# Performance work log

Measured on AMD Instinct MI355X. Metric: run time of the kernel, lower is better.

## Reference

```python
import jax, jax.numpy as jnp
import numpy as np

B, S, E, R = 64, 2048, 256, 50


def setup_inputs() -> dict:
    key = jax.random.key(0)
    ks = jax.random.split(key, 22)
    n = lambda k, shp, s=0.05: (jax.random.normal(k, shp, jnp.float32) * s)
    d = {
        "encoder_o": jax.random.normal(ks[0], (B, S, E), jnp.float32),
        "h0": jax.random.normal(ks[1], (1, B, E), jnp.float32),
        "c0": jax.random.normal(ks[2], (1, B, E), jnp.float32),
        "r_in": jax.random.randint(ks[3], (B,), 0, R),
        "k1": jax.random.randint(ks[4], (B, 1), 0, S),
        "k2": jax.random.randint(ks[5], (B, 1), 0, S),
        "W_ih": n(ks[6], (4 * E, E)),
        "W_hh": n(ks[7], (4 * E, E)),
        "b_ih": n(ks[8], (4 * E,)),
        "b_hh": n(ks[9], (4 * E,)),
        "W_attn": n(ks[10], (E, 2 * E)),
        "b_attn": n(ks[11], (E,)),
        "W_conv": n(ks[12], (E, 2 * E, 3)),
        "b_conv": n(ks[13], (E,)),
        "sos_emb": n(ks[14], (1, E)),
        "rel_emb": n(ks[15], (R, E)),
        "W_rel": n(ks[16], (R, E)),
        "b_rel": n(ks[17], (R,)),
        "W_ent1": n(ks[18], (1, E)),
        "b_ent1": n(ks[19], (1,)),
        "W_ent2": n(ks[20], (1, E)),
        "b_ent2": n(ks[21], (1,)),
    }
    return d


def reference(encoder_o, h0, c0, r_in, k1, k2, W_ih, W_hh, b_ih, b_hh,
              W_attn, b_attn, W_conv, b_conv, sos_emb, rel_emb,
              W_rel, b_rel, W_ent1, b_ent1, W_ent2, b_ent2):
    Bx, Sx, Ex = encoder_o.shape

    def lstm_step(x, h, c):  # single decode step, x/h/c: [B,E]
        gates = x @ W_ih.T + h @ W_hh.T + (b_ih + b_hh)  # [B,4E]
        i, f, g, o = jnp.split(gates, 4, axis=-1)        # PyTorch gate order i,f,g,o
        c2 = jax.nn.sigmoid(f) * c + jax.nn.sigmoid(i) * jnp.tanh(g)
        h2 = jax.nn.sigmoid(o) * jnp.tanh(c2)
        return h2, c2

    def attend(q):  # Luong dot attention + tanh(linear(cat(mix,q))); q: [B,E]
        scores = jnp.einsum('be,bse->bs', q, encoder_o)
        attn = jax.nn.softmax(scores, axis=-1)
        mix = jnp.einsum('bs,bse->be', attn, encoder_o)
        comb = jnp.concatenate([mix, q], axis=-1)        # [B,2E]
        return jnp.tanh(comb @ W_attn.T + b_attn)

    def step(x, h, c):
        h2, c2 = lstm_step(x, h, c)
        return attend(h2), h2, c2

    kern = jnp.transpose(W_conv, (2, 1, 0))  # [3, 2E, E] for NWC/WIO

    def ent_heads(o):  # o: [B,E]
        vec = jnp.broadcast_to(o[:, None, :], (Bx, Sx, Ex))  # seq_and_vec
        feat = jnp.concatenate([encoder_o, vec], axis=-1)    # [B,S,2E]
        conv = jax.lax.conv_general_dilated(
            feat, kern, (1,), 'SAME',
            dimension_numbers=('NWC', 'WIO', 'NWC')) + b_conv
        conv = jax.nn.relu(conv)                             # [B,S,E]
        e1 = conv @ W_ent1.T + b_ent1                        # [B,S,1]
        e2 = conv @ W_ent2.T + b_ent2
        return e1, e2

    h, c = h0[0], c0[0]
    # t1: <sos> -> relation logits
    x = jnp.broadcast_to(sos_emb[0], (Bx, Ex))
    out1, h, c = step(x, h, c)
    t1_out = out1 @ W_rel.T + b_rel                          # [B,R]
    # t2: relation embedding -> entity-1 span heads
    out2, h, c = step(rel_emb[r_in], h, c)
    e1a, e2a = ent_heads(out2)
    # t3: gathered k1+k2 encoder vectors -> entity-2 span heads
    idx = jnp.arange(Bx)
    kk = encoder_o[idx, k1[:, 0]] + encoder_o[idx, k2[:, 0]]  # vectorized seq_gather
    out3, h, c = step(kk, h, c)
    e1b, e2b = ent_heads(out3)
    # pack outputs: [B, R + 4*S]
    return jnp.concatenate(
        [t1_out, e1a[..., 0], e2a[..., 0], e1b[..., 0], e2b[..., 0]], axis=1)
```

## Files before the change

### kernel.cpp

```cpp
#include <hip/hip_runtime.h>
#include <hip/hip_bf16.h>

#define EE 256
#define SS 2048
#define BB 64
#define RN 50
#define OSTR 8242
#define NCH 16

typedef __attribute__((ext_vector_type(4))) float vf4;
typedef __attribute__((ext_vector_type(8))) short s8v;
typedef __attribute__((ext_vector_type(4))) short s4v;
typedef __attribute__((ext_vector_type(4))) unsigned short u16x4;
typedef __attribute__((ext_vector_type(2))) unsigned int u32x2;
typedef __attribute__((ext_vector_type(4))) unsigned int u32x4;

__device__ __forceinline__ unsigned short f2bf(float f){
  __hip_bfloat16 h = __float2bfloat16(f);
  return *reinterpret_cast<unsigned short*>(&h);
}
__device__ __forceinline__ unsigned int f2bf2(float a, float b){
  __hip_bfloat162 h = __float22bfloat162_rn(make_float2(a, b));
  return *reinterpret_cast<unsigned int*>(&h);
}
__device__ __forceinline__ float sigm(float x){ return 1.0f/(1.0f + __expf(-x)); }
__device__ __forceinline__ float dot4(vf4 a, vf4 b){ return a.x*b.x + a.y*b.y + a.z*b.z + a.w*b.w; }

__device__ __forceinline__ vf4 mfma16(s4v a, s4v b, vf4 c){
#if __has_builtin(__builtin_amdgcn_mfma_f32_16x16x16bf16_1k)
  return __builtin_amdgcn_mfma_f32_16x16x16bf16_1k(a, b, c, 0, 0, 0);
#else
  vf4 d;
  asm volatile("v_mfma_f32_16x16x16_bf16 %0, %1, %2, %3\n\ts_nop 7\n\ts_nop 7"
               : "=v"(d) : "v"(a), "v"(b), "v"(c));
  return d;
#endif
}

__device__ __forceinline__ void gload_lds16(const void* g, void* l){
  __builtin_amdgcn_global_load_lds(
      (const __attribute__((address_space(1))) unsigned int*)g,
      (__attribute__((address_space(3))) unsigned int*)l, 16, 0, 0);
}

__global__ __launch_bounds__(256) void k_prep(
  const float* __restrict__ enc, const float* __restrict__ h0, const float* __restrict__ c0,
  const int* __restrict__ r_in, const int* __restrict__ k1, const int* __restrict__ k2,
  const float* __restrict__ sos, const float* __restrict__ rel,
  const float* __restrict__ W_conv,
  float* __restrict__ xT, float* __restrict__ hT0, float* __restrict__ cT,
  unsigned short* __restrict__ WT, unsigned short* __restrict__ Bp)
{
  int bid = blockIdx.x, t = threadIdx.x;
  if (bid < 256){
    int part = bid >> 6, b = bid & 63;
    if (part == 0){
      xT[(size_t)0*EE*BB + t*BB + b] = sos[t];
    } else if (part == 1){
      xT[(size_t)1*EE*BB + t*BB + b] = rel[r_in[b]*EE + t];
    } else if (part == 2){
      int i1 = k1[b], i2 = k2[b];
      xT[(size_t)2*EE*BB + t*BB + b] =
        enc[((size_t)b*SS + i1)*EE + t] + enc[((size_t)b*SS + i2)*EE + t];
    } else {
      hT0[t*BB + b] = h0[b*EE + t];
      cT [t*BB + b] = c0[b*EE + t];
    }
  } else if (bid < 512){
    int o = bid - 256;
    for (int r = t; r < 768; r += 256)
      WT[(size_t)r*EE + o] = f2bf(W_conv[(size_t)o*1536 + 768 + r]);
  } else {
    int gid = (bid - 512)*256 + t;
    int kc  = gid >> 10;
    int rem = gid & 1023;
    int ni  = rem >> 6;
    int l   = rem & 63;
    int o   = ni*16 + (l & 15);
    int kbase = kc*32 + ((l >> 4) << 3);
    u16x4 lo4, hi4;
    #pragma unroll
    for (int j=0;j<8;++j){
      int k = kbase + j; int ktap = k >> 8; int i = k & 255;
      unsigned short v = f2bf(W_conv[((size_t)o*512 + i)*3 + ktap]);
      if (j<4){ if(j==0)lo4.x=v; else if(j==1)lo4.y=v; else if(j==2)lo4.z=v; else lo4.w=v; }
      else    { if(j==4)hi4.x=v; else if(j==5)hi4.y=v; else if(j==6)hi4.z=v; else hi4.w=v; }
    }
    u16x4* dst = (u16x4*)(Bp + (size_t)gid*8);
    dst[0] = lo4; dst[1] = hi4;
  }
}

__global__ __launch_bounds__(1024) void k_step(
  const float* __restrict__ hT_cur, const float* __restrict__ xT_st,
  const float* __restrict__ W_ih, const float* __restrict__ W_hh,
  const float* __restrict__ b_ih, const float* __restrict__ b_hh,
  float* __restrict__ cT, float* __restrict__ hT_next, float* __restrict__ hs_st)
{
  int e = blockIdx.x, tid = threadIdx.x;
  int w = tid >> 6, b = tid & 63;
  int g = w & 3, kq = w >> 2;
  int grow = g*EE + e;
  const float* wh = W_hh + (size_t)grow*EE + kq*64;
  const float* wi = W_ih + (size_t)grow*EE + kq*64;
  const float* hT = hT_cur + kq*64*BB;
  const float* xv = xT_st + kq*64*BB;
  float acc = (kq == 0) ? (b_ih[grow] + b_hh[grow]) : 0.0f;
  #pragma unroll 4
  for (int k4 = 0; k4 < 16; ++k4){
    vf4 wh4 = *(const vf4*)(wh + k4*4);
    vf4 wi4 = *(const vf4*)(wi + k4*4);
    int k = k4*4;
    acc += hT[(k+0)*BB+b]*wh4.x + hT[(k+1)*BB+b]*wh4.y
         + hT[(k+2)*BB+b]*wh4.z + hT[(k+3)*BB+b]*wh4.w;
    acc += xv[(k+0)*BB+b]*wi4.x + xv[(k+1)*BB+b]*wi4.y
         + xv[(k+2)*BB+b]*wi4.z + xv[(k+3)*BB+b]*wi4.w;
  }
  __shared__ float sm[16][BB];
  sm[w][b] = acc;
  __syncthreads();
  if (tid < BB){
    float iv = sm[0][tid]+sm[4][tid]+sm[8][tid] +sm[12][tid];
    float fv = sm[1][tid]+sm[5][tid]+sm[9][tid] +sm[13][tid];
    float gv = sm[2][tid]+sm[6][tid]+sm[10][tid]+sm[14][tid];
    float ov = sm[3][tid]+sm[7][tid]+sm[11][tid]+sm[15][tid];
    float cprev = cT[e*BB + tid];
    float cn = sigm(fv)*cprev + sigm(iv)*tanhf(gv);
    float hn = sigm(ov)*tanhf(cn);
    cT[e*BB + tid] = cn;
    hT_next[e*BB + tid] = hn;
    hs_st[(size_t)tid*EE + e] = hn;
  }
}

__global__ __launch_bounds__(256) void k_attend(
  const float* __restrict__ enc, const float* __restrict__ hs,
  float* __restrict__ mixc, float* __restrict__ stats,
  unsigned short* __restrict__ encb)
{
  int bid = blockIdx.x; int b = bid >> 4, ch = bid & 15;
  int tid = threadIdx.x, lane = tid & 63, wv = tid >> 6;
  __shared__ float sc[3][128];
  __shared__ vf4 mpart[4][3][64];

  const float* chunk = enc + ((size_t)b*SS + ch*128)*EE;

  {
    int rs = lane >> 4, cg = lane & 15;
    vf4 q0[4], q1[4], q2[4];
    #pragma unroll
    for (int v=0; v<4; ++v){
      q0[v] = *(const vf4*)(hs + ((size_t)0*BB + b)*EE + cg*16 + v*4);
      q1[v] = *(const vf4*)(hs + ((size_t)1*BB + b)*EE + cg*16 + v*4);
      q2[v] = *(const vf4*)(hs + ((size_t)2*BB + b)*EE + cg*16 + v*4);
    }
    #pragma unroll
    for (int i=0; i<8; ++i){
      int r = wv*32 + i*4 + rs;
      const vf4* rp = (const vf4*)(chunk + (size_t)r*EE + cg*16);
      vf4 e0v = rp[0], e1v = rp[1], e2v = rp[2], e3v = rp[3];
      float a0 = dot4(e0v,q0[0]) + dot4(e1v,q0[1]) + dot4(e2v,q0[2]) + dot4(e3v,q0[3]);
      float a1 = dot4(e0v,q1[0]) + dot4(e1v,q1[1]) + dot4(e2v,q1[2]) + dot4(e3v,q1[3]);
      float a2 = dot4(e0v,q2[0]) + dot4(e1v,q2[1]) + dot4(e2v,q2[2]) + dot4(e3v,q2[3]);
      if (encb){
        int gs = ch*128 + r;
        int key = ((gs + 1) & 7) << 4;
        char* base = (char*)encb + ((size_t)b*SS + gs)*512;
        u32x4 p1; p1.x = f2bf2(e0v.x,e0v.y); p1.y = f2bf2(e0v.z,e0v.w);
                  p1.z = f2bf2(e1v.x,e1v.y); p1.w = f2bf2(e1v.z,e1v.w);
        u32x4 p2; p2.x = f2bf2(e2v.x,e2v.y); p2.y = f2bf2(e2v.z,e2v.w);
                  p2.z = f2bf2(e3v.x,e3v.y); p2.w = f2bf2(e3v.z,e3v.w);
        *(u32x4*)(base + ((cg*32     ) ^ key)) = p1;
        *(u32x4*)(base + ((cg*32 + 16) ^ key)) = p2;
      }
      #pragma unroll
      for (int d=1; d<16; d<<=1){
        a0 += __shfl_xor(a0,d); a1 += __shfl_xor(a1,d); a2 += __shfl_xor(a2,d);
      }
      if (cg == 0){ sc[0][r]=a0; sc[1][r]=a1; sc[2][r]=a2; }
    }
  }
  __syncthreads();

  if (tid < 64){
    float s0a = sc[0][tid], s0b = sc[0][64+tid];
    float s1a = sc[1][tid], s1b = sc[1][64+tid];
    float s2a = sc[2][tid], s2b = sc[2][64+tid];
    float m0 = fmaxf(s0a,s0b), m1 = fmaxf(s1a,s1b), m2 = fmaxf(s2a,s2b);
    #pragma unroll
    for (int d=1; d<64; d<<=1){
      m0 = fmaxf(m0, __shfl_xor(m0,d));
      m1 = fmaxf(m1, __shfl_xor(m1,d));
      m2 = fmaxf(m2, __shfl_xor(m2,d));
    }
    float e0a = __expf(s0a-m0), e0b = __expf(s0b-m0);
    float e1a = __expf(s1a-m1), e1b = __expf(s1b-m1);
    float e2a = __expf(s2a-m2), e2b = __expf(s2b-m2);
    sc[0][tid]=e0a; sc[0][64+tid]=e0b;
    sc[1][tid]=e1a; sc[1][64+tid]=e1b;
    sc[2][tid]=e2a; sc[2][64+tid]=e2b;
    float l0=e0a+e0b, l1=e1a+e1b, l2=e2a+e2b;
    #pragma unroll
    for (int d=1; d<64; d<<=1){
      l0 += __shfl_xor(l0,d); l1 += __shfl_xor(l1,d); l2 += __shfl_xor(l2,d);
    }
    if (tid == 0){
      int o0 = ((0*BB+b)*NCH + ch)*2; stats[o0]=m0; stats[o0+1]=l0;
      int o1 = ((1*BB+b)*NCH + ch)*2; stats[o1]=m1; stats[o1+1]=l1;
      int o2 = ((2*BB+b)*NCH + ch)*2; stats[o2]=m2; stats[o2+1]=l2;
    }
  }
  __syncthreads();

  {
    vf4 A0 = (vf4)0.0f, A1 = (vf4)0.0f, A2 = (vf4)0.0f;
    #pragma unroll 4
    for (int j=0;j<32;++j){
      int r = wv*32 + j;
      int gs = ch*128 + r;
      vf4 ev;
      if (encb){
        int key = ((gs + 1) & 7) << 4;
        u32x2 pk = *(const u32x2*)((const char*)encb + ((size_t)b*SS + gs)*512 + ((lane*8) ^ key));
        ev.x = __uint_as_float(pk.x << 16);
        ev.y = __uint_as_float(pk.x & 0xFFFF0000u);
        ev.z = __uint_as_float(pk.y << 16);
        ev.w = __uint_as_float(pk.y & 0xFFFF0000u);
      } else {
        ev = *(const vf4*)(chunk + (size_t)r*EE + lane*4);
      }
      float w0 = sc[0][r], w1 = sc[1][r], w2 = sc[2][r];
      A0 += ev*w0; A1 += ev*w1; A2 += ev*w2;
    }
    mpart[wv][0][lane]=A0; mpart[wv][1][lane]=A1; mpart[wv][2][lane]=A2;
  }
  __syncthreads();
  if (tid < 192){
    int q = tid >> 6, e4 = tid & 63;
    vf4 sum = mpart[0][q][e4] + mpart[1][q][e4] + mpart[2][q][e4] + mpart[3][q][e4];
    *(vf4*)(mixc + ((size_t)(q*BB+b)*NCH + ch)*EE + e4*4) = sum;
  }
}

__global__ __launch_bounds__(256) void k_post(
  const float* __restrict__ mixc, const float* __restrict__ hs,
  const float* __restrict__ stats,
  const float* __restrict__ W_attn, const float* __restrict__ b_attn,
  const float* __restrict__ W_rel, const float* __restrict__ b_rel,
  const unsigned short* __restrict__ WT, const float* __restrict__ b_conv,
  float* __restrict__ out, float* __restrict__ vv)
{
  int b = blockIdx.x, t = threadIdx.x;
  __shared__ float comb[3][2*EE];
  __shared__ float o1[EE], o2s[EE], o3s[EE];
  #pragma unroll
  for (int q=0;q<3;q++){
    float M = -1e30f;
    for (int c=0;c<NCH;c++) M = fmaxf(M, stats[((q*BB+b)*NCH + c)*2]);
    float L = 0.f, macc = 0.f;
    for (int c=0;c<NCH;c++){
      int o = ((q*BB+b)*NCH + c)*2;
      float e = __expf(stats[o]-M);
      L += stats[o+1]*e;
      macc += mixc[((size_t)(q*BB+b)*NCH + c)*EE + t] * e;
    }
    comb[q][t] = macc / L;
    comb[q][EE+t] = hs[((size_t)q*BB + b)*EE + t];
  }
  __syncthreads();
  float a0 = b_attn[t], a1 = a0, a2 = a0;
  const vf4* wr = (const vf4*)(W_attn + (size_t)t*2*EE);
  const vf4* c0v = (const vf4*)comb[0];
  const vf4* c1v = (const vf4*)comb[1];
  const vf4* c2v = (const vf4*)comb[2];
  #pragma unroll 4
  for (int k=0;k<2*EE/4;++k){
    vf4 w = wr[k];
    a0 += dot4(w, c0v[k]); a1 += dot4(w, c1v[k]); a2 += dot4(w, c2v[k]);
  }
  o1[t]=tanhf(a0); o2s[t]=tanhf(a1); o3s[t]=tanhf(a2);
  __syncthreads();
  if (t < RN){
    float acc = b_rel[t];
    const vf4* wrel = (const vf4*)(W_rel + (size_t)t*EE);
    const vf4* ov = (const vf4*)o1;
    for (int k=0;k<EE/4;++k) acc += dot4(wrel[k], ov[k]);
    out[(size_t)b*OSTR + t] = acc;
  }
  float va0=0,va1=0,va2=0, vb0=0,vb1=0,vb2=0;
  for (int i=0;i<EE;++i){
    float x2 = o2s[i], x3 = o3s[i];
    const unsigned short* wt = WT + (size_t)i*3*EE + t;
    float w0 = __uint_as_float(((unsigned int)wt[0]) << 16);
    float w1 = __uint_as_float(((unsigned int)wt[EE]) << 16);
    float w2 = __uint_as_float(((unsigned int)wt[2*EE]) << 16);
    va0 += x2*w0; va1 += x2*w1; va2 += x2*w2;
    vb0 += x3*w0; vb1 += x3*w1; vb2 += x3*w2;
  }
  float bc = b_conv[t];
  vv[((0*3+0)*BB + b)*EE + t] = va0+va1+va2+bc;
  vv[((0*3+1)*BB + b)*EE + t] = va1+va2+bc;
  vv[((0*3+2)*BB + b)*EE + t] = va0+va1+bc;
  vv[((1*3+0)*BB + b)*EE + t] = vb0+vb1+vb2+bc;
  vv[((1*3+1)*BB + b)*EE + t] = vb1+vb2+bc;
  vv[((1*3+2)*BB + b)*EE + t] = vb0+vb1+bc;
}

__global__ __launch_bounds__(256, 3) void k_conv(
  const float* __restrict__ enc, const unsigned short* __restrict__ encb,
  const unsigned short* __restrict__ Bp,
  const float* __restrict__ vv,
  const float* __restrict__ W_e1, const float* __restrict__ b_e1,
  const float* __restrict__ W_e2, const float* __restrict__ b_e2,
  float* __restrict__ out)
{
  int stile = blockIdx.x, b = blockIdx.y;
  int s0 = stile*64;
  int tid = threadIdx.x, lane = tid & 63, w = tid >> 6;
  int lo = lane & 15, hi = lane >> 4;
  __shared__ __align__(16) unsigned short Ab[66*256];
  __shared__ float part2[4][64][4];

  if (encb){
    const char* ebase = (const char*)encb + (size_t)b*SS*512;
    for (int base = 0; base < 66*32; base += 256){
      int idx = base + tid;
      if (idx < 66*32){
        int r = idx >> 5, c = idx & 31;
        int srow = s0 - 1 + r;
        srow = srow < 0 ? 0 : (srow > SS-1 ? SS-1 : srow);
        gload_lds16(ebase + (size_t)srow*512 + c*16, (char*)Ab + idx*16);
      }
    }
    __syncthreads();
    if (stile == 0 || stile == 31){
      if (stile == 0  && tid < 32) *(vf4*)((char*)Ab + tid*16) = (vf4)0.0f;
      if (stile == 31 && tid < 32) *(vf4*)((char*)Ab + 65*512 + tid*16) = (vf4)0.0f;
      __syncthreads();
    }
  } else {
    const float* eb = enc + (size_t)b*SS*EE;
    for (int idx = tid; idx < 66*64; idx += 256){
      int r = idx >> 6, c4 = idx & 63;
      int s = s0 - 1 + r;
      vf4 v = (vf4)0.0f;
      if (s >= 0 && s < SS) v = *(const vf4*)(eb + (size_t)s*EE + c4*4);
      u32x2 pk; pk.x = f2bf2(v.x, v.y); pk.y = f2bf2(v.z, v.w);
      int byte = (r*512 + c4*8) ^ ((r & 7) << 4);
      *(u32x2*)((char*)Ab + byte) = pk;
    }
    __syncthreads();
  }

  vf4 acc[4][4];
  #pragma unroll
  for (int oi=0;oi<4;++oi){
    #pragma unroll
    for (int si=0;si<4;++si) acc[oi][si] = (vf4)0.0f;
  }
  const s8v* Bp8 = (const s8v*)Bp;
  s8v bf[4], bfn[4];
  #pragma unroll
  for (int oi=0;oi<4;++oi) bf[oi] = Bp8[((0*16 + (w*4+oi)) << 6) + lane];

  for (int kc=0; kc<24; ++kc){
    int ktap = kc >> 3;
    int colb = ((kc & 7) << 6) + (hi << 4);
    s8v af[4];
    #pragma unroll
    for (int si=0;si<4;++si){
      int row = si*16 + lo + ktap;
      int byte = row*512 + (colb ^ ((row & 7) << 4));
      af[si] = *(const s8v*)((const char*)Ab + byte);
    }
    if (kc < 23){
      #pragma unroll
      for (int oi=0;oi<4;++oi) bfn[oi] = Bp8[(((kc+1)*16 + (w*4+oi)) << 6) + lane];
    }
    #pragma unroll
    for (int oi=0;oi<4;++oi){
      #pragma unroll
      for (int si=0;si<4;++si)
        acc[oi][si] = __builtin_amdgcn_mfma_f32_16x16x32_bf16(bf[oi], af[si], acc[oi][si], 0, 0, 0);
    }
    #pragma unroll
    for (int oi=0;oi<4;++oi) bf[oi] = bfn[oi];
  }

  bool firstTile = (s0 == 0), lastTile = (s0 + 64 == SS);
  vf4 vaI[4], vbI[4]; s4v aw[4];
  #pragma unroll
  for (int oi=0;oi<4;++oi){
    int o4 = w*64 + oi*16 + hi*4;
    vaI[oi] = *(const vf4*)(vv + ((0*3+0)*BB + b)*EE + o4);
    vbI[oi] = *(const vf4*)(vv + ((1*3+0)*BB + b)*EE + o4);
    vf4 w1 = *(const vf4*)(W_e1 + o4);
    vf4 w2 = *(const vf4*)(W_e2 + o4);
    float e0 = (lo==0) ? w1.x : ((lo==1) ? w2.x : 0.0f);
    float e1 = (lo==0) ? w1.y : ((lo==1) ? w2.y : 0.0f);
    float e2 = (lo==0) ? w1.z : ((lo==1) ? w2.z : 0.0f);
    float e3 = (lo==0) ? w1.w : ((lo==1) ? w2.w : 0.0f);
    u32x2 t; t.x = f2bf2(e0, e1); t.y = f2bf2(e2, e3);
    aw[oi] = __builtin_bit_cast(s4v, t);
  }
  #pragma unroll
  for (int si=0; si<4; ++si){
    vf4 Da = (vf4)0.0f, Db = (vf4)0.0f;
    #pragma unroll
    for (int oi=0; oi<4; ++oi){
      int o4 = w*64 + oi*16 + hi*4;
      vf4 c = acc[oi][si];
      vf4 va = vaI[oi], vb = vbI[oi];
      if (firstTile && si==0 && lo==0){
        va = *(const vf4*)(vv + ((0*3+1)*BB + b)*EE + o4);
        vb = *(const vf4*)(vv + ((1*3+1)*BB + b)*EE + o4);
      }
      if (lastTile && si==3 && lo==15){
        va = *(const vf4*)(vv + ((0*3+2)*BB + b)*EE + o4);
        vb = *(const vf4*)(vv + ((1*3+2)*BB + b)*EE + o4);
      }
      float a0 = fmaxf(c.x+va.x,0.f), a1 = fmaxf(c.y+va.y,0.f);
      float a2 = fmaxf(c.z+va.z,0.f), a3 = fmaxf(c.w+va.w,0.f);
      float b0 = fmaxf(c.x+vb.x,0.f), b1 = fmaxf(c.y+vb.y,0.f);
      float b2 = fmaxf(c.z+vb.z,0.f), b3 = fmaxf(c.w+vb.w,0.f);
      u32x2 ta; ta.x = f2bf2(a0,a1); ta.y = f2bf2(a2,a3);
      u32x2 tb; tb.x = f2bf2(b0,b1); tb.y = f2bf2(b2,b3);
      Da = mfma16(aw[oi], __builtin_bit_cast(s4v, ta), Da);
      Db = mfma16(aw[oi], __builtin_bit_cast(s4v, tb), Db);
    }
    if (hi == 0){
      vf4 pk; pk.x = Da.x; pk.y = Da.y; pk.z = Db.x; pk.w = Db.y;
      *(vf4*)&part2[w][si*16+lo][0] = pk;
    }
  }
  __syncthreads();
  {
    int s = tid >> 2, c = tid & 3;
    float r = part2[0][s][c] + part2[1][s][c] + part2[2][s][c] + part2[3][s][c];
    r += (c & 1) ? b_e2[0] : b_e1[0];
    out[(size_t)b*OSTR + RN + c*SS + (s0 + s)] = r;
  }
}

extern "C" void kernel_launch(void* const* d_in, const int* in_sizes, int n_in,
                              void* d_out, int out_size, void* d_ws, size_t ws_size,
                              hipStream_t stream)
{
  const float* enc   = (const float*)d_in[0];
  const float* h0    = (const float*)d_in[1];
  const float* c0    = (const float*)d_in[2];
  const int*   r_in  = (const int*)d_in[3];
  const int*   k1    = (const int*)d_in[4];
  const int*   k2    = (const int*)d_in[5];
  const float* W_ih  = (const float*)d_in[6];
  const float* W_hh  = (const float*)d_in[7];
  const float* b_ih  = (const float*)d_in[8];
  const float* b_hh  = (const float*)d_in[9];
  const float* W_attn= (const float*)d_in[10];
  const float* b_attn= (const float*)d_in[11];
  const float* W_conv= (const float*)d_in[12];
  const float* b_conv= (const float*)d_in[13];
  const float* sos   = (const float*)d_in[14];
  const float* rel   = (const float*)d_in[15];
  const float* W_rel = (const float*)d_in[16];
  const float* b_rel = (const float*)d_in[17];
  const float* W_e1  = (const float*)d_in[18];
  const float* b_e1  = (const float*)d_in[19];
  const float* W_e2  = (const float*)d_in[20];
  const float* b_e2  = (const float*)d_in[21];
  float* out = (float*)d_out;
  char* ws = (char*)d_ws;

  float* hs    = (float*)(ws);
  float* vv    = (float*)(ws + 196608);
  float* stats = (float*)(ws + 589824);
  float* mixc  = (float*)(ws + 638976);
  unsigned short* Bp = (unsigned short*)(ws + 6930432);
  float* xT    = (float*)(ws + 7323648);
  float* hTa   = (float*)(ws + 7520256);
  float* hTb   = (float*)(ws + 7585792);
  float* cT    = (float*)(ws + 7651328);
  unsigned short* WT = (unsigned short*)(ws + 7716864);
  size_t encb_off = 8110080;
  size_t need = encb_off + (size_t)BB*SS*EE*2;
  unsigned short* encb = (ws_size >= need) ? (unsigned short*)(ws + encb_off) : nullptr;

  hipLaunchKernelGGL(k_prep,  dim3(608), dim3(256), 0, stream,
                     enc,h0,c0,r_in,k1,k2,sos,rel,W_conv, xT,hTa,cT, WT,Bp);
  hipLaunchKernelGGL(k_step,  dim3(256), dim3(1024), 0, stream,
                     hTa, xT + 0*EE*BB, W_ih,W_hh,b_ih,b_hh, cT, hTb, hs + 0*BB*EE);
  hipLaunchKernelGGL(k_step,  dim3(256), dim3(1024), 0, stream,
                     hTb, xT + 1*EE*BB, W_ih,W_hh,b_ih,b_hh, cT, hTa, hs + 1*BB*EE);
  hipLaunchKernelGGL(k_step,  dim3(256), dim3(1024), 0, stream,
                     hTa, xT + 2*EE*BB, W_ih,W_hh,b_ih,b_hh, cT, hTb, hs + 2*BB*EE);
  hipLaunchKernelGGL(k_attend,dim3(1024), dim3(256), 0, stream, enc, hs, mixc, stats, encb);
  hipLaunchKernelGGL(k_post,  dim3(64),  dim3(256), 0, stream,
                     mixc, hs, stats, W_attn,b_attn, W_rel,b_rel, WT, b_conv, out, vv);
  hipLaunchKernelGGL(k_conv,  dim3(32,64), dim3(256), 0, stream,
                     enc, encb, Bp, vv, W_e1,b_e1, W_e2,b_e2, out);
}
```

Baseline: 183.9 us.

## Split attention kernel into separate score and mix kernels

Splits the fused attention kernel into two kernels. The first computes the three query scores per position and writes them, together with the bf16 swizzled encoder copy, to global memory. The second reads the scores back, does the chunk softmax, and accumulates the mix from the bf16 copy. This removes the in-block barrier between scoring and mixing, but adds a kernel launch, a global round trip for the scores, and a second pass over the encoder data, which may now miss in cache.

```diff
diff --git a/kernel.cpp b/kernel.cpp
--- a/kernel.cpp
+++ b/kernel.cpp
@@ -133,59 +133,73 @@
   }
 }
 
-__global__ __launch_bounds__(256) void k_attend(
+__global__ __launch_bounds__(256) void k_score(
   const float* __restrict__ enc, const float* __restrict__ hs,
+  float* __restrict__ scw, unsigned short* __restrict__ encb)
+{
+  int bid = blockIdx.x; int b = bid >> 4, wg = bid & 15;
+  int tid = threadIdx.x, lane = tid & 63, wv = tid >> 6;
+  int rs = lane >> 4, cg = lane & 15;
+  int s0 = (wg*4 + wv)*32;
+  const float* chunk = enc + ((size_t)b*SS + s0)*EE;
+
+  vf4 q0[4], q1[4], q2[4];
+  #pragma unroll
+  for (int v=0; v<4; ++v){
+    q0[v] = *(const vf4*)(hs + ((size_t)0*BB + b)*EE + cg*16 + v*4);
+    q1[v] = *(const vf4*)(hs + ((size_t)1*BB + b)*EE + cg*16 + v*4);
+    q2[v] = *(const vf4*)(hs + ((size_t)2*BB + b)*EE + cg*16 + v*4);
+  }
+  #pragma unroll
+  for (int i=0; i<8; ++i){
+    int r = i*4 + rs;
+    const vf4* rp = (const vf4*)(chunk + (size_t)r*EE + cg*16);
+    vf4 e0v = rp[0], e1v = rp[1], e2v = rp[2], e3v = rp[3];
+    float a0 = dot4(e0v,q0[0]) + dot4(e1v,q0[1]) + dot4(e2v,q0[2]) + dot4(e3v,q0[3]);
+    float a1 = dot4(e0v,q1[0]) + dot4(e1v,q1[1]) + dot4(e2v,q1[2]) + dot4(e3v,q1[3]);
+    float a2 = dot4(e0v,q2[0]) + dot4(e1v,q2[1]) + dot4(e2v,q2[2]) + dot4(e3v,q2[3]);
+    if (encb){
+      int gs = s0 + r;
+      int key = ((gs + 1) & 7) << 4;
+      char* base = (char*)encb + ((size_t)b*SS + gs)*512;
+      u32x4 p1; p1.x = f2bf2(e0v.x,e0v.y); p1.y = f2bf2(e0v.z,e0v.w);
+                p1.z = f2bf2(e1v.x,e1v.y); p1.w = f2bf2(e1v.z,e1v.w);
+      u32x4 p2; p2.x = f2bf2(e2v.x,e2v.y); p2.y = f2bf2(e2v.z,e2v.w);
+                p2.z = f2bf2(e3v.x,e3v.y); p2.w = f2bf2(e3v.z,e3v.w);
+      *(u32x4*)(base + ((cg*32     ) ^ key)) = p1;
+      *(u32x4*)(base + ((cg*32 + 16) ^ key)) = p2;
+    }
+    #pragma unroll
+    for (int d=1; d<16; d<<=1){
+      a0 += __shfl_xor(a0,d); a1 += __shfl_xor(a1,d); a2 += __shfl_xor(a2,d);
+    }
+    if (cg == 0){
+      int s = s0 + r;
+      scw[((size_t)0*BB + b)*SS + s] = a0;
+      scw[((size_t)1*BB + b)*SS + s] = a1;
+      scw[((size_t)2*BB + b)*SS + s] = a2;
+    }
+  }
+}
+
+__global__ __launch_bounds__(256) void k_mix(
+  const float* __restrict__ enc, const float* __restrict__ scw,
   float* __restrict__ mixc, float* __restrict__ stats,
-  unsigned short* __restrict__ encb)
+  const unsigned short* __restrict__ encb)
 {
   int bid = blockIdx.x; int b = bid >> 4, ch = bid & 15;
   int tid = threadIdx.x, lane = tid & 63, wv = tid >> 6;
   __shared__ float sc[3][128];
   __shared__ vf4 mpart[4][3][64];
 
-  const float* chunk = enc + ((size_t)b*SS + ch*128)*EE;
-
-  {
-    int rs = lane >> 4, cg = lane & 15;
-    vf4 q0[4], q1[4], q2[4];
-    #pragma unroll
-    for (int v=0; v<4; ++v){
-      q0[v] = *(const vf4*)(hs + ((size_t)0*BB + b)*EE + cg*16 + v*4);
-      q1[v] = *(const vf4*)(hs + ((size_t)1*BB + b)*EE + cg*16 + v*4);
-      q2[v] = *(const vf4*)(hs + ((size_t)2*BB + b)*EE + cg*16 + v*4);
-    }
-    #pragma unroll
-    for (int i=0; i<8; ++i){
-      int r = wv*32 + i*4 + rs;
-      const vf4* rp = (const vf4*)(chunk + (size_t)r*EE + cg*16);
-      vf4 e0v = rp[0], e1v = rp[1], e2v = rp[2], e3v = rp[3];
-      float a0 = dot4(e0v,q0[0]) + dot4(e1v,q0[1]) + dot4(e2v,q0[2]) + dot4(e3v,q0[3]);
-      float a1 = dot4(e0v,q1[0]) + dot4(e1v,q1[1]) + dot4(e2v,q1[2]) + dot4(e3v,q1[3]);
-      float a2 = dot4(e0v,q2[0]) + dot4(e1v,q2[1]) + dot4(e2v,q2[2]) + dot4(e3v,q2[3]);
-      if (encb){
-        int gs = ch*128 + r;
-        int key = ((gs + 1) & 7) << 4;
-        char* base = (char*)encb + ((size_t)b*SS + gs)*512;
-        u32x4 p1; p1.x = f2bf2(e0v.x,e0v.y); p1.y = f2bf2(e0v.z,e0v.w);
-                  p1.z = f2bf2(e1v.x,e1v.y); p1.w = f2bf2(e1v.z,e1v.w);
-        u32x4 p2; p2.x = f2bf2(e2v.x,e2v.y); p2.y = f2bf2(e2v.z,e2v.w);
-                  p2.z = f2bf2(e3v.x,e3v.y); p2.w = f2bf2(e3v.z,e3v.w);
-        *(u32x4*)(base + ((cg*32     ) ^ key)) = p1;
-        *(u32x4*)(base + ((cg*32 + 16) ^ key)) = p2;
-      }
-      #pragma unroll
-      for (int d=1; d<16; d<<=1){
-        a0 += __shfl_xor(a0,d); a1 += __shfl_xor(a1,d); a2 += __shfl_xor(a2,d);
-      }
-      if (cg == 0){ sc[0][r]=a0; sc[1][r]=a1; sc[2][r]=a2; }
-    }
-  }
-  __syncthreads();
-
   if (tid < 64){
-    float s0a = sc[0][tid], s0b = sc[0][64+tid];
-    float s1a = sc[1][tid], s1b = sc[1][64+tid];
-    float s2a = sc[2][tid], s2b = sc[2][64+tid];
+    int sbase = ch*128 + tid;
+    float s0a = scw[((size_t)0*BB + b)*SS + sbase];
+    float s0b = scw[((size_t)0*BB + b)*SS + sbase + 64];
+    float s1a = scw[((size_t)1*BB + b)*SS + sbase];
+    float s1b = scw[((size_t)1*BB + b)*SS + sbase + 64];
+    float s2a = scw[((size_t)2*BB + b)*SS + sbase];
+    float s2b = scw[((size_t)2*BB + b)*SS + sbase + 64];
     float m0 = fmaxf(s0a,s0b), m1 = fmaxf(s1a,s1b), m2 = fmaxf(s2a,s2b);
     #pragma unroll
     for (int d=1; d<64; d<<=1){
@@ -227,7 +241,7 @@
         ev.z = __uint_as_float(pk.y << 16);
         ev.w = __uint_as_float(pk.y & 0xFFFF0000u);
       } else {
-        ev = *(const vf4*)(chunk + (size_t)r*EE + lane*4);
+        ev = *(const vf4*)(enc + ((size_t)b*SS + gs)*EE + lane*4);
       }
       float w0 = sc[0][r], w1 = sc[1][r], w2 = sc[2][r];
       A0 += ev*w0; A1 += ev*w1; A2 += ev*w2;
@@ -475,6 +489,7 @@
   float* vv    = (float*)(ws + 196608);
   float* stats = (float*)(ws + 589824);
   float* mixc  = (float*)(ws + 638976);
+  float* scw   = (float*)(ws + 3784704);
   unsigned short* Bp = (unsigned short*)(ws + 6930432);
   float* xT    = (float*)(ws + 7323648);
   float* hTa   = (float*)(ws + 7520256);
@@ -493,7 +508,8 @@
                      hTb, xT + 1*EE*BB, W_ih,W_hh,b_ih,b_hh, cT, hTa, hs + 1*BB*EE);
   hipLaunchKernelGGL(k_step,  dim3(256), dim3(1024), 0, stream,
                      hTa, xT + 2*EE*BB, W_ih,W_hh,b_ih,b_hh, cT, hTb, hs + 2*BB*EE);
-  hipLaunchKernelGGL(k_attend,dim3(1024), dim3(256), 0, stream, enc, hs, mixc, stats, encb);
+  hipLaunchKernelGGL(k_score, dim3(1024), dim3(256), 0, stream, enc, hs, scw, encb);
+  hipLaunchKernelGGL(k_mix,   dim3(1024), dim3(256), 0, stream, enc, scw, mixc, stats, encb);
   hipLaunchKernelGGL(k_post,  dim3(64),  dim3(256), 0, stream,
                      mixc, hs, stats, W_attn,b_attn, W_rel,b_rel, WT, b_conv, out, vv);
   hipLaunchKernelGGL(k_conv,  dim3(32,64), dim3(256), 0, stream,
```

New measurement: 188.0 us. +2.3%, slower.

## Give each wave its own attention chunk and drop block-level syncs

Applied to the files above, without the earlier changes.

The attention kernel now gives each 64-lane wave its own independent 64-row chunk of the sequence. Doubling the chunk count (NCH 16→32) lets every wave compute scores, a local softmax and its partial mix without any __syncthreads or cross-wave reduction through shared memory. The mix pass now rereads the fp32 encoder rows the same wave just loaded, which should still be in cache, instead of the bf16 copy. The cost is twice as many partial mix/stat records for the post kernel to merge, a larger mixc buffer in the workspace, and more read bytes in the second pass.

```diff
diff --git a/kernel.cpp b/kernel.cpp
--- a/kernel.cpp
+++ b/kernel.cpp
@@ -6,7 +6,7 @@
 #define BB 64
 #define RN 50
 #define OSTR 8242
-#define NCH 16
+#define NCH 32
 
 typedef __attribute__((ext_vector_type(4))) float vf4;
 typedef __attribute__((ext_vector_type(8))) short s8v;
@@ -138,107 +138,82 @@
   float* __restrict__ mixc, float* __restrict__ stats,
   unsigned short* __restrict__ encb)
 {
-  int bid = blockIdx.x; int b = bid >> 4, ch = bid & 15;
+  int bid = blockIdx.x; int b = bid >> 3, grp = bid & 7;
   int tid = threadIdx.x, lane = tid & 63, wv = tid >> 6;
-  __shared__ float sc[3][128];
-  __shared__ vf4 mpart[4][3][64];
-
-  const float* chunk = enc + ((size_t)b*SS + ch*128)*EE;
+  int ch = grp*4 + wv;
+  int rs = lane >> 4, cg = lane & 15;
+  __shared__ float sc[4][3][64];
+
+  const float* chunk = enc + ((size_t)b*SS + ch*64)*EE;
+
+  vf4 q0[4], q1[4], q2[4];
+  #pragma unroll
+  for (int v=0; v<4; ++v){
+    q0[v] = *(const vf4*)(hs + ((size_t)0*BB + b)*EE + cg*16 + v*4);
+    q1[v] = *(const vf4*)(hs + ((size_t)1*BB + b)*EE + cg*16 + v*4);
+    q2[v] = *(const vf4*)(hs + ((size_t)2*BB + b)*EE + cg*16 + v*4);
+  }
+
+  #pragma unroll
+  for (int i=0; i<16; ++i){
+    int r = i*4 + rs;
+    const vf4* rp = (const vf4*)(chunk + (size_t)r*EE + cg*16);
+    vf4 e0v = rp[0], e1v = rp[1], e2v = rp[2], e3v = rp[3];
+    float a0 = dot4(e0v,q0[0]) + dot4(e1v,q0[1]) + dot4(e2v,q0[2]) + dot4(e3v,q0[3]);
+    float a1 = dot4(e0v,q1[0]) + dot4(e1v,q1[1]) + dot4(e2v,q1[2]) + dot4(e3v,q1[3]);
+    float a2 = dot4(e0v,q2[0]) + dot4(e1v,q2[1]) + dot4(e2v,q2[2]) + dot4(e3v,q2[3]);
+    if (encb){
+      int gs = ch*64 + r;
+      int key = ((gs + 1) & 7) << 4;
+      char* base = (char*)encb + ((size_t)b*SS + gs)*512;
+      u32x4 p1; p1.x = f2bf2(e0v.x,e0v.y); p1.y = f2bf2(e0v.z,e0v.w);
+                p1.z = f2bf2(e1v.x,e1v.y); p1.w = f2bf2(e1v.z,e1v.w);
+      u32x4 p2; p2.x = f2bf2(e2v.x,e2v.y); p2.y = f2bf2(e2v.z,e2v.w);
+                p2.z = f2bf2(e3v.x,e3v.y); p2.w = f2bf2(e3v.z,e3v.w);
+      *(u32x4*)(base + ((cg*32     ) ^ key)) = p1;
+      *(u32x4*)(base + ((cg*32 + 16) ^ key)) = p2;
+    }
+    #pragma unroll
+    for (int d=1; d<16; d<<=1){
+      a0 += __shfl_xor(a0,d); a1 += __shfl_xor(a1,d); a2 += __shfl_xor(a2,d);
+    }
+    if (cg == 0){ sc[wv][0][r]=a0; sc[wv][1][r]=a1; sc[wv][2][r]=a2; }
+  }
 
   {
-    int rs = lane >> 4, cg = lane & 15;
-    vf4 q0[4], q1[4], q2[4];
-    #pragma unroll
-    for (int v=0; v<4; ++v){
-      q0[v] = *(const vf4*)(hs + ((size_t)0*BB + b)*EE + cg*16 + v*4);
-      q1[v] = *(const vf4*)(hs + ((size_t)1*BB + b)*EE + cg*16 + v*4);
-      q2[v] = *(const vf4*)(hs + ((size_t)2*BB + b)*EE + cg*16 + v*4);
-    }
-    #pragma unroll
-    for (int i=0; i<8; ++i){
-      int r = wv*32 + i*4 + rs;
-      const vf4* rp = (const vf4*)(chunk + (size_t)r*EE + cg*16);
-      vf4 e0v = rp[0], e1v = rp[1], e2v = rp[2], e3v = rp[3];
-      float a0 = dot4(e0v,q0[0]) + dot4(e1v,q0[1]) + dot4(e2v,q0[2]) + dot4(e3v,q0[3]);
-      float a1 = dot4(e0v,q1[0]) + dot4(e1v,q1[1]) + dot4(e2v,q1[2]) + dot4(e3v,q1[3]);
-      float a2 = dot4(e0v,q2[0]) + dot4(e1v,q2[1]) + dot4(e2v,q2[2]) + dot4(e3v,q2[3]);
-      if (encb){
-        int gs = ch*128 + r;
-        int key = ((gs + 1) & 7) << 4;
-        char* base = (char*)encb + ((size_t)b*SS + gs)*512;
-        u32x4 p1; p1.x = f2bf2(e0v.x,e0v.y); p1.y = f2bf2(e0v.z,e0v.w);
-                  p1.z = f2bf2(e1v.x,e1v.y); p1.w = f2bf2(e1v.z,e1v.w);
-        u32x4 p2; p2.x = f2bf2(e2v.x,e2v.y); p2.y = f2bf2(e2v.z,e2v.w);
-                  p2.z = f2bf2(e3v.x,e3v.y); p2.w = f2bf2(e3v.z,e3v.w);
-        *(u32x4*)(base + ((cg*32     ) ^ key)) = p1;
-        *(u32x4*)(base + ((cg*32 + 16) ^ key)) = p2;
-      }
-      #pragma unroll
-      for (int d=1; d<16; d<<=1){
-        a0 += __shfl_xor(a0,d); a1 += __shfl_xor(a1,d); a2 += __shfl_xor(a2,d);
-      }
-      if (cg == 0){ sc[0][r]=a0; sc[1][r]=a1; sc[2][r]=a2; }
-    }
-  }
-  __syncthreads();
-
-  if (tid < 64){
-    float s0a = sc[0][tid], s0b = sc[0][64+tid];
-    float s1a = sc[1][tid], s1b = sc[1][64+tid];
-    float s2a = sc[2][tid], s2b = sc[2][64+tid];
-    float m0 = fmaxf(s0a,s0b), m1 = fmaxf(s1a,s1b), m2 = fmaxf(s2a,s2b);
+    float s0 = sc[wv][0][lane], s1 = sc[wv][1][lane], s2 = sc[wv][2][lane];
+    float m0=s0, m1=s1, m2=s2;
     #pragma unroll
     for (int d=1; d<64; d<<=1){
       m0 = fmaxf(m0, __shfl_xor(m0,d));
       m1 = fmaxf(m1, __shfl_xor(m1,d));
       m2 = fmaxf(m2, __shfl_xor(m2,d));
     }
-    float e0a = __expf(s0a-m0), e0b = __expf(s0b-m0);
-    float e1a = __expf(s1a-m1), e1b = __expf(s1b-m1);
-    float e2a = __expf(s2a-m2), e2b = __expf(s2b-m2);
-    sc[0][tid]=e0a; sc[0][64+tid]=e0b;
-    sc[1][tid]=e1a; sc[1][64+tid]=e1b;
-    sc[2][tid]=e2a; sc[2][64+tid]=e2b;
-    float l0=e0a+e0b, l1=e1a+e1b, l2=e2a+e2b;
+    float e0 = __expf(s0-m0), e1 = __expf(s1-m1), e2 = __expf(s2-m2);
+    sc[wv][0][lane]=e0; sc[wv][1][lane]=e1; sc[wv][2][lane]=e2;
+    float l0=e0, l1=e1, l2=e2;
     #pragma unroll
     for (int d=1; d<64; d<<=1){
       l0 += __shfl_xor(l0,d); l1 += __shfl_xor(l1,d); l2 += __shfl_xor(l2,d);
     }
-    if (tid == 0){
+    if (lane == 0){
       int o0 = ((0*BB+b)*NCH + ch)*2; stats[o0]=m0; stats[o0+1]=l0;
       int o1 = ((1*BB+b)*NCH + ch)*2; stats[o1]=m1; stats[o1+1]=l1;
       int o2 = ((2*BB+b)*NCH + ch)*2; stats[o2]=m2; stats[o2+1]=l2;
     }
   }
-  __syncthreads();
 
   {
     vf4 A0 = (vf4)0.0f, A1 = (vf4)0.0f, A2 = (vf4)0.0f;
-    #pragma unroll 4
-    for (int j=0;j<32;++j){
-      int r = wv*32 + j;
-      int gs = ch*128 + r;
-      vf4 ev;
-      if (encb){
-        int key = ((gs + 1) & 7) << 4;
-        u32x2 pk = *(const u32x2*)((const char*)encb + ((size_t)b*SS + gs)*512 + ((lane*8) ^ key));
-        ev.x = __uint_as_float(pk.x << 16);
-        ev.y = __uint_as_float(pk.x & 0xFFFF0000u);
-        ev.z = __uint_as_float(pk.y << 16);
-        ev.w = __uint_as_float(pk.y & 0xFFFF0000u);
-      } else {
-        ev = *(const vf4*)(chunk + (size_t)r*EE + lane*4);
-      }
-      float w0 = sc[0][r], w1 = sc[1][r], w2 = sc[2][r];
+    #pragma unroll 8
+    for (int r=0; r<64; ++r){
+      vf4 ev = *(const vf4*)(chunk + (size_t)r*EE + lane*4);
+      float w0 = sc[wv][0][r], w1 = sc[wv][1][r], w2 = sc[wv][2][r];
       A0 += ev*w0; A1 += ev*w1; A2 += ev*w2;
     }
-    mpart[wv][0][lane]=A0; mpart[wv][1][lane]=A1; mpart[wv][2][lane]=A2;
-  }
-  __syncthreads();
-  if (tid < 192){
-    int q = tid >> 6, e4 = tid & 63;
-    vf4 sum = mpart[0][q][e4] + mpart[1][q][e4] + mpart[2][q][e4] + mpart[3][q][e4];
-    *(vf4*)(mixc + ((size_t)(q*BB+b)*NCH + ch)*EE + e4*4) = sum;
+    *(vf4*)(mixc + ((size_t)(0*BB+b)*NCH + ch)*EE + lane*4) = A0;
+    *(vf4*)(mixc + ((size_t)(1*BB+b)*NCH + ch)*EE + lane*4) = A1;
+    *(vf4*)(mixc + ((size_t)(2*BB+b)*NCH + ch)*EE + lane*4) = A2;
   }
 }
 
@@ -493,7 +468,7 @@
                      hTb, xT + 1*EE*BB, W_ih,W_hh,b_ih,b_hh, cT, hTa, hs + 1*BB*EE);
   hipLaunchKernelGGL(k_step,  dim3(256), dim3(1024), 0, stream,
                      hTa, xT + 2*EE*BB, W_ih,W_hh,b_ih,b_hh, cT, hTb, hs + 2*BB*EE);
-  hipLaunchKernelGGL(k_attend,dim3(1024), dim3(256), 0, stream, enc, hs, mixc, stats, encb);
+  hipLaunchKernelGGL(k_attend,dim3(512), dim3(256), 0, stream, enc, hs, mixc, stats, encb);
   hipLaunchKernelGGL(k_post,  dim3(64),  dim3(256), 0, stream,
                      mixc, hs, stats, W_attn,b_attn, W_rel,b_rel, WT, b_conv, out, vv);
   hipLaunchKernelGGL(k_conv,  dim3(32,64), dim3(256), 0, stream,
```

Result: slower. 195.4 us (+6.3%).
